# Kernel optimization log

Measured on AMD Instinct MI355X. Metric: run time of the kernel, lower is better.

## Reference

```python
import jax, jax.numpy as jnp
import numpy as np

B, S, E, D, H = 32, 4096, 512, 512, 512


def setup_inputs() -> dict:
    key = jax.random.key(0)
    ks = jax.random.split(key, 7)
    scale = 1.0 / np.sqrt(H)
    return {
        "encoder_hiddens": jax.random.normal(ks[0], (B, S, E), dtype=jnp.float32),
        "decoder_hidden": jax.random.normal(ks[1], (B, D), dtype=jnp.float32),
        "W_enc": jax.random.uniform(ks[2], (H, E), jnp.float32, -scale, scale),
        "b_enc": jax.random.uniform(ks[3], (H,), jnp.float32, -scale, scale),
        "W_dec": jax.random.uniform(ks[4], (H, D), jnp.float32, -scale, scale),
        "b_dec": jax.random.uniform(ks[5], (H,), jnp.float32, -scale, scale),
        "v": jax.random.uniform(ks[6], (H,), jnp.float32, -scale, scale),
    }


def reference(encoder_hiddens, decoder_hidden, W_enc, b_enc, W_dec, b_dec, v):
    # Projections (the two small GEMMs of the original per-timestep loop, batched)
    enc_hs = jnp.einsum("bse,he->bsh", encoder_hiddens, W_enc) + b_enc  # [B,S,H]
    dec_h = decoder_hidden @ W_dec.T + b_dec                            # [B,H]

    # Ragged-length detection: the torch loop breaks at the first all-zero
    # projected encoder row; positions at/after that are excluded (cumulative AND).
    nonzero = jnp.any(enc_hs != 0, axis=-1)                             # [B,S]
    valid = jnp.cumprod(nonzero.astype(jnp.int32), axis=1).astype(bool)

    # Additive (Bahdanau) scores: v . tanh(enc_hs + dec_h)
    scores = jnp.einsum("h,bsh->bs", v, jnp.tanh(enc_hs + dec_h[:, None, :]))
    scores = jnp.where(valid, scores, -jnp.inf)
    attn = jax.nn.softmax(scores, axis=1)                               # [B,S]
    attn = jnp.where(valid, attn, 0.0)

    # Weighted sum of encoder states -> context vector [B,1,E]
    return jnp.sum(encoder_hiddens * attn[..., None], axis=1, keepdims=True)
```

## Files before the change

### kernel.cpp

```cpp
#include <hip/hip_runtime.h>
#include <hip/hip_bf16.h>

#define BATCH 32
#define SEQ   4096
#define EDIM  512
#define HDIM  512
#define NCHUNK 64
#define NBLK  (BATCH * NCHUNK)

typedef unsigned short u16;
typedef unsigned int   u32;

typedef __bf16 bf16x8 __attribute__((ext_vector_type(8)));
typedef float  f32x4  __attribute__((ext_vector_type(4)));

__device__ __forceinline__ u16 bf_rne(float x) {
    u32 u = __float_as_uint(x);
    u32 r = (u + 0x7fffu + ((u >> 16) & 1u)) >> 16;
    return (u16)r;
}
__device__ __forceinline__ u32 pack2(u16 lo, u16 hi) {
    return (u32)lo | ((u32)hi << 16);
}
__device__ __forceinline__ float tanh_fast(float x) {
    float e = __builtin_amdgcn_exp2f(x * 2.88539008177793f);
    return 1.0f - 2.0f * __builtin_amdgcn_rcpf(e + 1.0f);
}

__global__ void prep_kernel(const float* __restrict__ W_enc, uint4* __restrict__ wpack,
                            const float* __restrict__ dec, const float* __restrict__ Wd,
                            const float* __restrict__ b_enc, const float* __restrict__ b_dec,
                            float* __restrict__ dec_bias) {
    int bid = blockIdx.x;
    int t = threadIdx.x;
    if (bid < 4096) {
        int wave = t >> 6, lane = t & 63;
        int p = bid * 4 + wave;
        int b = p >> 9, h = p & 511;
        const float4* wr = reinterpret_cast<const float4*>(Wd)  + h * 128;
        const float4* dr = reinterpret_cast<const float4*>(dec) + b * 128;
        float4 w0 = wr[lane * 2], w1 = wr[lane * 2 + 1];
        float4 d0 = dr[lane * 2], d1 = dr[lane * 2 + 1];
        float s = w0.x * d0.x + w0.y * d0.y + w0.z * d0.z + w0.w * d0.w
                + w1.x * d1.x + w1.y * d1.y + w1.z * d1.z + w1.w * d1.w;
#pragma unroll
        for (int m = 1; m < 64; m <<= 1) s += __shfl_xor(s, m, 64);
        if (lane == 0) dec_bias[p] = s + b_dec[h] + b_enc[h];
    } else {
        int id   = (bid - 4096) * 256 + t;
        int nsub = id >> 10;
        int rem  = id & 1023;
        int kc   = rem >> 6;
        int lane = rem & 63;
        int row  = nsub * 16 + (lane & 15);
        int col  = kc * 32 + (lane >> 4) * 8;
        const float* src = W_enc + row * EDIM + col;
        uint4 o;
        o.x = pack2(bf_rne(src[0]), bf_rne(src[1]));
        o.y = pack2(bf_rne(src[2]), bf_rne(src[3]));
        o.z = pack2(bf_rne(src[4]), bf_rne(src[5]));
        o.w = pack2(bf_rne(src[6]), bf_rne(src[7]));
        wpack[id] = o;
    }
}

__global__ __launch_bounds__(256, 2) void fused_kernel(
    const float* __restrict__ X, const uint4* __restrict__ Wp,
    const float* __restrict__ bias, const float* __restrict__ v,
    float* __restrict__ cpart, float* __restrict__ mpart, float* __restrict__ lpart)
{
    __shared__ alignas(16) u16 Abuf[2][64 * 72];
    __shared__ float sred[4][64];
    __shared__ float pbuf[64];

    const int tid  = threadIdx.x;
    const int wave = tid >> 6, lane = tid & 63;
    const int quad = lane >> 4, l15 = lane & 15;
    const int blk  = blockIdx.x;
    const int b    = blk >> 6;
    const long row0 = (long)blk * 64;
    const float4* X4 = reinterpret_cast<const float4*>(X + row0 * EDIM);

    f32x4 acc[4][8] = {};

    const int r  = tid >> 2;
    const int c8 = tid & 3;

    float4 pA = X4[r * 128 + c8 * 2];
    float4 pB = X4[r * 128 + c8 * 2 + 1];
    {
        uint4 w;
        w.x = pack2(bf_rne(pA.x), bf_rne(pA.y));
        w.y = pack2(bf_rne(pA.z), bf_rne(pA.w));
        w.z = pack2(bf_rne(pB.x), bf_rne(pB.y));
        w.w = pack2(bf_rne(pB.z), bf_rne(pB.w));
        *reinterpret_cast<uint4*>(&Abuf[0][r * 72 + c8 * 8]) = w;
    }
    pA = X4[r * 128 + 8 + c8 * 2];
    pB = X4[r * 128 + 8 + c8 * 2 + 1];
    __syncthreads();

    for (int ch = 0; ch < 16; ch++) {
        const u16* Ab = Abuf[ch & 1];

        uint4 braw[8];
#pragma unroll
        for (int jj = 0; jj < 8; jj++)
            braw[jj] = Wp[((wave * 8 + jj) * 16 + ch) * 64 + lane];

        float4 nA, nB;
        if (ch < 14) {
            nA = X4[r * 128 + (ch + 2) * 8 + c8 * 2];
            nB = X4[r * 128 + (ch + 2) * 8 + c8 * 2 + 1];
        }

        bf16x8 af[4];
#pragma unroll
        for (int i = 0; i < 4; i++)
            af[i] = *reinterpret_cast<const bf16x8*>(&Ab[(i * 16 + l15) * 72 + quad * 8]);
#pragma unroll
        for (int jj = 0; jj < 8; jj++) {
            bf16x8 bfr = __builtin_bit_cast(bf16x8, braw[jj]);
#pragma unroll
            for (int i = 0; i < 4; i++)
                acc[i][jj] = __builtin_amdgcn_mfma_f32_16x16x32_bf16(
                    af[i], bfr, acc[i][jj], 0, 0, 0);
        }

        if (ch < 15) {
            uint4 w;
            w.x = pack2(bf_rne(pA.x), bf_rne(pA.y));
            w.y = pack2(bf_rne(pA.z), bf_rne(pA.w));
            w.z = pack2(bf_rne(pB.x), bf_rne(pB.y));
            w.w = pack2(bf_rne(pB.z), bf_rne(pB.w));
            *reinterpret_cast<uint4*>(&Abuf[(ch & 1) ^ 1][r * 72 + c8 * 8]) = w;
        }
        __syncthreads();
        if (ch < 14) { pA = nA; pB = nB; }
    }

    float hb[8], hv[8];
#pragma unroll
    for (int jj = 0; jj < 8; jj++) {
        int h = wave * 128 + jj * 16 + l15;
        hb[jj] = bias[b * HDIM + h];
        hv[jj] = v[h];
    }
    float s_acc[16];
#pragma unroll
    for (int x = 0; x < 16; x++) s_acc[x] = 0.f;
#pragma unroll
    for (int i = 0; i < 4; i++)
#pragma unroll
        for (int jj = 0; jj < 8; jj++)
#pragma unroll
            for (int rr = 0; rr < 4; rr++)
                s_acc[i * 4 + rr] += hv[jj] * tanh_fast(acc[i][jj][rr] + hb[jj]);

#pragma unroll
    for (int m = 1; m < 16; m <<= 1)
#pragma unroll
        for (int x = 0; x < 16; x++)
            s_acc[x] += __shfl_xor(s_acc[x], m, 16);

    if (l15 == 0) {
#pragma unroll
        for (int x = 0; x < 16; x++) {
            int i = x >> 2, rr = x & 3;
            sred[wave][i * 16 + quad * 4 + rr] = s_acc[x];
        }
    }
    __syncthreads();

    if (tid < 64) {
        float sc = sred[0][tid] + sred[1][tid] + sred[2][tid] + sred[3][tid];
        float mx = sc;
#pragma unroll
        for (int m = 1; m < 64; m <<= 1) mx = fmaxf(mx, __shfl_xor(mx, m, 64));
        float p = __builtin_amdgcn_exp2f((sc - mx) * 1.44269504088896f);
        float l = p;
#pragma unroll
        for (int m = 1; m < 64; m <<= 1) l += __shfl_xor(l, m, 64);
        pbuf[tid] = p;
        if (tid == 0) { mpart[blk] = mx; lpart[blk] = l; }
    }
    __syncthreads();

    const float2* Xp = reinterpret_cast<const float2*>(X + row0 * EDIM) + tid;
    float ax0 = 0.f, ay0 = 0.f, ax1 = 0.f, ay1 = 0.f;
#pragma unroll 2
    for (int s = 0; s < 64; s += 8) {
        float2 x[8];
#pragma unroll
        for (int k = 0; k < 8; k++) x[k] = Xp[(s + k) * 256];
#pragma unroll
        for (int k = 0; k < 8; k += 2) {
            float w0 = pbuf[s + k], w1 = pbuf[s + k + 1];
            ax0 = fmaf(w0, x[k].x,     ax0);
            ay0 = fmaf(w0, x[k].y,     ay0);
            ax1 = fmaf(w1, x[k + 1].x, ax1);
            ay1 = fmaf(w1, x[k + 1].y, ay1);
        }
    }
    reinterpret_cast<float2*>(cpart)[blk * 256 + tid] =
        make_float2(ax0 + ax1, ay0 + ay1);
}

__global__ __launch_bounds__(256) void combine_k(const float* __restrict__ cpart,
                                                 const float* __restrict__ mpart,
                                                 const float* __restrict__ lpart,
                                                 float* __restrict__ out) {
    __shared__ float wbuf[64];
    __shared__ float linv_s;
    int b = blockIdx.x, t = threadIdx.x;
    if (t < 64) {
        float m = mpart[b * 64 + t];
        float M = m;
#pragma unroll
        for (int k = 1; k < 64; k <<= 1) M = fmaxf(M, __shfl_xor(M, k, 64));
        float w = __builtin_amdgcn_exp2f((m - M) * 1.44269504088896f);
        float lw = lpart[b * 64 + t] * w;
        float L = lw;
#pragma unroll
        for (int k = 1; k < 64; k <<= 1) L += __shfl_xor(L, k, 64);
        wbuf[t] = w;
        if (t == 0) linv_s = 1.0f / L;
    }
    __syncthreads();
    const float2* cp = reinterpret_cast<const float2*>(cpart) + (long)b * 64 * 256 + t;
    float ax = 0.f, ay = 0.f;
#pragma unroll 2
    for (int i = 0; i < 64; i += 8) {
        float2 x[8];
#pragma unroll
        for (int k = 0; k < 8; k++) x[k] = cp[(i + k) * 256];
#pragma unroll
        for (int k = 0; k < 8; k++) {
            float w = wbuf[i + k];
            ax = fmaf(w, x[k].x, ax);
            ay = fmaf(w, x[k].y, ay);
        }
    }
    float inv = linv_s;
    reinterpret_cast<float2*>(out)[b * 256 + t] = make_float2(ax * inv, ay * inv);
}

extern "C" void kernel_launch(void* const* d_in, const int* in_sizes, int n_in,
                              void* d_out, int out_size, void* d_ws, size_t ws_size,
                              hipStream_t stream) {
    const float* X      = (const float*)d_in[0];
    const float* dec    = (const float*)d_in[1];
    const float* W_enc  = (const float*)d_in[2];
    const float* b_enc  = (const float*)d_in[3];
    const float* W_dec  = (const float*)d_in[4];
    const float* b_dec  = (const float*)d_in[5];
    const float* v      = (const float*)d_in[6];
    float* out = (float*)d_out;

    char* ws = (char*)d_ws;
    uint4* wpack    = (uint4*)ws;
    float* dec_bias = (float*)(ws + (512 << 10));
    float* cpart    = (float*)(ws + (576 << 10));
    float* mpart    = (float*)(ws + (576 << 10) + (4096 << 10));
    float* lpart    = (float*)(ws + (576 << 10) + (4104 << 10));

    prep_kernel  <<<4224, 256, 0, stream>>>(W_enc, wpack, dec, W_dec, b_enc, b_dec,
                                            dec_bias);
    fused_kernel <<<NBLK, 256, 0, stream>>>(X, wpack, dec_bias, v, cpart, mpart, lpart);
    combine_k    <<<BATCH, 256, 0, stream>>>(cpart, mpart, lpart, out);
}
```

Baseline: 446.0 us.

## Stage full 64-row A tile in LDS upfront and drop per-chunk barriers

Replaces the double-buffered 32-column A pipeline with a single load phase: each thread issues 16 float4 loads per group, converts them to bf16, and writes the whole 64x512 tile into LDS with a padded stride. The k-loop then runs with no __syncthreads and register-prefetches the next chunk's packed weights. This removes 16 barriers per block and lets more global loads be in flight at once. In exchange, LDS per block grows to about 66KB, which may limit occupancy to the stated 2 blocks per CU or fewer. It also removes the overlap of X loading with MFMA work and raises register pressure.

```diff
diff --git a/kernel.cpp b/kernel.cpp
--- a/kernel.cpp
+++ b/kernel.cpp
@@ -64,12 +64,14 @@
     }
 }
 
+#define ASTRIDE 520
+
 __global__ __launch_bounds__(256, 2) void fused_kernel(
     const float* __restrict__ X, const uint4* __restrict__ Wp,
     const float* __restrict__ bias, const float* __restrict__ v,
     float* __restrict__ cpart, float* __restrict__ mpart, float* __restrict__ lpart)
 {
-    __shared__ alignas(16) u16 Abuf[2][64 * 72];
+    __shared__ alignas(16) u16 Abuf[64 * ASTRIDE];
     __shared__ float sred[4][64];
     __shared__ float pbuf[64];
 
@@ -81,62 +83,62 @@
     const long row0 = (long)blk * 64;
     const float4* X4 = reinterpret_cast<const float4*>(X + row0 * EDIM);
 
-    f32x4 acc[4][8] = {};
-
     const int r  = tid >> 2;
     const int c8 = tid & 3;
 
-    float4 pA = X4[r * 128 + c8 * 2];
-    float4 pB = X4[r * 128 + c8 * 2 + 1];
-    {
-        uint4 w;
-        w.x = pack2(bf_rne(pA.x), bf_rne(pA.y));
-        w.y = pack2(bf_rne(pA.z), bf_rne(pA.w));
-        w.z = pack2(bf_rne(pB.x), bf_rne(pB.y));
-        w.w = pack2(bf_rne(pB.z), bf_rne(pB.w));
-        *reinterpret_cast<uint4*>(&Abuf[0][r * 72 + c8 * 8]) = w;
-    }
-    pA = X4[r * 128 + 8 + c8 * 2];
-    pB = X4[r * 128 + 8 + c8 * 2 + 1];
-    __syncthreads();
-
-    for (int ch = 0; ch < 16; ch++) {
-        const u16* Ab = Abuf[ch & 1];
-
-        uint4 braw[8];
-#pragma unroll
-        for (int jj = 0; jj < 8; jj++)
-            braw[jj] = Wp[((wave * 8 + jj) * 16 + ch) * 64 + lane];
-
-        float4 nA, nB;
-        if (ch < 14) {
-            nA = X4[r * 128 + (ch + 2) * 8 + c8 * 2];
-            nB = X4[r * 128 + (ch + 2) * 8 + c8 * 2 + 1];
-        }
-
+#pragma unroll
+    for (int g = 0; g < 2; g++) {
+        float4 st[16];
+#pragma unroll
+        for (int p = 0; p < 8; p++) {
+            int piece = (g * 8 + p) * 4 + c8;
+            st[2 * p]     = X4[r * 128 + piece * 2];
+            st[2 * p + 1] = X4[r * 128 + piece * 2 + 1];
+        }
+#pragma unroll
+        for (int p = 0; p < 8; p++) {
+            int piece = (g * 8 + p) * 4 + c8;
+            uint4 w;
+            w.x = pack2(bf_rne(st[2 * p].x),     bf_rne(st[2 * p].y));
+            w.y = pack2(bf_rne(st[2 * p].z),     bf_rne(st[2 * p].w));
+            w.z = pack2(bf_rne(st[2 * p + 1].x), bf_rne(st[2 * p + 1].y));
+            w.w = pack2(bf_rne(st[2 * p + 1].z), bf_rne(st[2 * p + 1].w));
+            *reinterpret_cast<uint4*>(&Abuf[r * ASTRIDE + piece * 8]) = w;
+        }
+    }
+
+    f32x4 acc[4][8] = {};
+    __syncthreads();
+
+    uint4 bcur[8], bnxt[8];
+#pragma unroll
+    for (int jj = 0; jj < 8; jj++)
+        bcur[jj] = Wp[((wave * 8 + jj) * 16 + 0) * 64 + lane];
+
+#pragma unroll
+    for (int ks = 0; ks < 16; ks++) {
+        if (ks < 15) {
+#pragma unroll
+            for (int jj = 0; jj < 8; jj++)
+                bnxt[jj] = Wp[((wave * 8 + jj) * 16 + ks + 1) * 64 + lane];
+        }
         bf16x8 af[4];
 #pragma unroll
         for (int i = 0; i < 4; i++)
-            af[i] = *reinterpret_cast<const bf16x8*>(&Ab[(i * 16 + l15) * 72 + quad * 8]);
+            af[i] = *reinterpret_cast<const bf16x8*>(
+                &Abuf[(i * 16 + l15) * ASTRIDE + ks * 32 + quad * 8]);
 #pragma unroll
         for (int jj = 0; jj < 8; jj++) {
-            bf16x8 bfr = __builtin_bit_cast(bf16x8, braw[jj]);
+            bf16x8 bfr = __builtin_bit_cast(bf16x8, bcur[jj]);
 #pragma unroll
             for (int i = 0; i < 4; i++)
                 acc[i][jj] = __builtin_amdgcn_mfma_f32_16x16x32_bf16(
                     af[i], bfr, acc[i][jj], 0, 0, 0);
         }
-
-        if (ch < 15) {
-            uint4 w;
-            w.x = pack2(bf_rne(pA.x), bf_rne(pA.y));
-            w.y = pack2(bf_rne(pA.z), bf_rne(pA.w));
-            w.z = pack2(bf_rne(pB.x), bf_rne(pB.y));
-            w.w = pack2(bf_rne(pB.z), bf_rne(pB.w));
-            *reinterpret_cast<uint4*>(&Abuf[(ch & 1) ^ 1][r * 72 + c8 * 8]) = w;
-        }
-        __syncthreads();
-        if (ch < 14) { pA = nA; pB = nB; }
+        if (ks < 15) {
+#pragma unroll
+            for (int jj = 0; jj < 8; jj++) bcur[jj] = bnxt[jj];
+        }
     }
 
     float hb[8], hv[8];
```

Result: no change. 454.4 us (+1.9%).
